# Kernel tuning notes

Hardware: AMD Instinct MI355X
Metric: run time of the kernel (lower is better)

Reference implementation:

```python
import jax, jax.numpy as jnp
import numpy as np

T = 1 << 20          # sequence length
THRESHOLD = 1e-4     # decay-reset threshold (module default)


def setup_inputs() -> dict:
    key = jax.random.key(0)
    X = jax.random.normal(key, (T,), dtype=jnp.float32)
    # stable params near module init [0.2, 0.2, 0.0, 0.0]; small w3/w4 keep the
    # quadratic recurrence bounded while exercising all terms.
    params = jnp.array([0.2, 0.2, 0.05, 0.01], dtype=jnp.float32)
    return {"X": X, "params": params}


def reference(X, params):
    dt = X.dtype
    w1 = jnp.tanh(params[0]); dtanh1 = 1.0 - w1 * w1; d2tanh1 = -2.0 * w1 * dtanh1
    w2 = jnp.tanh(params[1]); dtanh2 = 1.0 - w2 * w2; d2tanh2 = -2.0 * w2 * dtanh2
    w3, w4 = params[2], params[3]

    def step(carry, x):
        h, Jh, Hh, decay = carry  # h:(), Jh:(4,), Hh:(4,4), decay:()
        h_new = w1 * x + w2 * h + w3 * x * x + w4 * h * h
        df_dw = jnp.stack([x * dtanh1, h * dtanh2, x * x, h * h])
        df_dh = w2 + 2.0 * w4 * h
        Jh_new = df_dw + df_dh * Jh
        Hww = (jnp.zeros((4, 4), dt)
               .at[0, 0].set(x * d2tanh1)
               .at[1, 1].set(h * d2tanh2))
        g = jnp.zeros((4,), dt).at[1].set(dtanh2).at[3].set(2.0 * h)
        outer = g[:, None] * Jh[None, :]
        Hh_new = Hww + outer + outer.T + df_dh * Hh
        decay_new = decay * jnp.abs(df_dh)
        reset = decay_new < THRESHOLD
        # torch zero_() mutates storage in-place, so the appended J/H entries at a
        # reset step are also zeroed -> emit post-reset values.
        Jh_out = jnp.where(reset, jnp.zeros((4,), dt), Jh_new)
        Hh_out = jnp.where(reset, jnp.zeros((4, 4), dt), Hh_new)
        h_out = jnp.where(reset, jax.lax.stop_gradient(h_new), h_new)  # detach
        decay_out = jnp.where(reset, jnp.ones((), dt), decay_new)
        return (h_out, Jh_out, Hh_out, decay_out), (h_new, Jh_out, Hh_out)

    init = (jnp.zeros((), dt), jnp.zeros((4,), dt), jnp.zeros((4, 4), dt),
            jnp.ones((), dt))
    _, (hs, Js, Hs) = jax.lax.scan(step, init, X[:-1])
    Z = jnp.concatenate([jnp.zeros((1,), dt), hs])              # [T]
    J = jnp.concatenate([jnp.zeros((1, 4), dt), Js])            # [T, 4]
    H = jnp.concatenate([jnp.zeros((1, 4, 4), dt), Hs])         # [T, 4, 4]
    return Z, J, H
```

## Files before the change

kernel.cpp:

```cpp
#include <hip/hip_runtime.h>
#include <math.h>

#define TLEN (1 << 20)
#define SB 32
#define NSB (TLEN / SB)
#define SCB 256
#define NSCB (NSB / SCB)
#define THRESH 1e-4f
#define IDMAP 0x00FAC688u

#define WWORDS (SCB * SB + 8)
#define WPAD(i) ((i) + ((i) >> 5))
#define LDSW WPAD(WWORDS)

#pragma clang fp contract(off)


#define CHUNK55(OFS, OUTARR) {                                                 \
        const float4* xp_ = (const float4*)(X + (OFS) - 24);                   \
        float xa_[56];                                                         \
        _Pragma("unroll")                                                      \
        for (int q_ = 0; q_ < 14; ++q_) {                                      \
            float4 v_ = xp_[q_];                                               \
            xa_[4 * q_ + 0] = v_.x; xa_[4 * q_ + 1] = v_.y;                    \
            xa_[4 * q_ + 2] = v_.z; xa_[4 * q_ + 3] = v_.w;                    \
        }                                                                      \
        float h_ = 0.0f;                                                       \
        _Pragma("unroll")                                                      \
        for (int p_ = 0; p_ < 55; ++p_) {                                      \
            float x_ = xa_[p_];                                                \
            float t1_ = w1 * x_;                                               \
            float t2_ = w2 * h_;                                               \
            float s1_ = t1_ + t2_;                                             \
            float t3_ = (w3 * x_) * x_;                                        \
            float s2_ = s1_ + t3_;                                             \
            float t4_ = (w4 * h_) * h_;                                        \
            h_ = s2_ + t4_;                                                    \
            if (p_ >= 23) OUTARR[p_ - 23] = h_;                                \
        }                                                                      \
    }

__global__ void __launch_bounds__(256) k_zts(const float* __restrict__ P,
                                             const float* __restrict__ X,
                                             float* __restrict__ c,
                                             float* __restrict__ Z,
                                             unsigned int* __restrict__ L32,
                                             unsigned int* __restrict__ BT,
                                             unsigned int* __restrict__ Msk) {
#pragma clang fp contract(off)
    __shared__ float sc[4];
    __shared__ float zw[LDSW];
    __shared__ unsigned int buf[2][SCB];
    int t = threadIdx.x;
    int b = blockIdx.x;
    if (t == 0) {
        float tw1 = (float)tanh((double)P[0]);
        float tw2 = (float)tanh((double)P[1]);
        sc[0] = tw1; sc[1] = tw2; sc[2] = P[2]; sc[3] = P[3];
        if (b == 0) {
            float dt1 = 1.0f - tw1 * tw1;
            float dt2 = 1.0f - tw2 * tw2;
            c[0] = tw1; c[1] = tw2; c[2] = P[2]; c[3] = P[3];
            c[4] = dt1; c[5] = dt2;
            c[6] = (-2.0f * tw1) * dt1; c[7] = (-2.0f * tw2) * dt2;
            c[8] = 2.0f * P[3];
        }
    }
    __syncthreads();
    float w1 = sc[0], w2 = sc[1], w3 = sc[2], w4 = sc[3];
    float w42 = 2.0f * w4;
    long gi = (long)b * SCB + t;
    long o = gi * 32;
    float out[32];
    if (gi == 0) {
        float h = 0.0f;
        out[0] = 0.0f;
        for (int k = 0; k < 31; ++k) {
            float x = X[k];
            float t1 = w1 * x;
            float t2 = w2 * h;
            float s1 = t1 + t2;
            float t3 = (w3 * x) * x;
            float s2 = s1 + t3;
            float t4 = (w4 * h) * h;
            h = s2 + t4;
            out[k + 1] = h;
        }
    } else {
        CHUNK55(o, out);
    }
#pragma unroll
    for (int q = 0; q < 8; ++q)
        *(float4*)(Z + o + 4 * q) = make_float4(out[4 * q], out[4 * q + 1],
                                                out[4 * q + 2], out[4 * q + 3]);
    int rbase = t * 32 + 8;
#pragma unroll
    for (int k = 0; k < 32; ++k) zw[WPAD(rbase + k)] = out[k];
    if (t == 0 && b > 0) {
        long op = (long)b * (SCB * SB) - 32;
        float pout[32];
        CHUNK55(op, pout);
#pragma unroll
        for (int q = 0; q < 7; ++q) zw[WPAD(1 + q)] = pout[25 + q];
    }
    __syncthreads();
    unsigned int m32;
    unsigned int msk[8];
    {
        float d[8]; int last[8];
#pragma unroll
        for (int g = 0; g < 8; ++g) { d[g] = 1.0f; last[g] = -g; msk[g] = 0u; }
        if (gi == 0) {
#pragma unroll
            for (int g = 0; g < 8; ++g) last[g] = 0;
            for (int k = 0; k < 32; ++k) {
                float fa = fabsf(w2 + w42 * zw[WPAD(rbase + k)]);
#pragma unroll
                for (int g = 0; g < 8; ++g) {
                    d[g] = d[g] * fa;
                    if (d[g] < THRESH) { last[g] = k + 1; d[g] = 1.0f; msk[g] |= 1u << k; }
                }
            }
        } else {
#pragma unroll
            for (int p = 0; p < 7; ++p) {
                float fa = fabsf(w2 + w42 * zw[WPAD(rbase + p - 7)]);
#pragma unroll
                for (int g = 7 - p; g < 8; ++g) {
                    d[g] = d[g] * fa;
                    if (d[g] < THRESH) { last[g] = p - 6; d[g] = 1.0f; }
                }
            }
            for (int k = 0; k < 32; ++k) {
                float fa = fabsf(w2 + w42 * zw[WPAD(rbase + k)]);
#pragma unroll
                for (int g = 0; g < 8; ++g) {
                    d[g] = d[g] * fa;
                    if (d[g] < THRESH) { last[g] = k + 1; d[g] = 1.0f; msk[g] |= 1u << k; }
                }
            }
        }
        if (gi < NSB - 1) {
            m32 = 0;
#pragma unroll
            for (int g = 0; g < 8; ++g) {
                int delta = 32 - last[g]; if (delta > 7) delta = 7;
                m32 |= (unsigned int)delta << (3 * g);
            }
        } else {
            m32 = IDMAP;
        }
    }
    uint4* mp = (uint4*)Msk + gi * 2;
    mp[0] = make_uint4(msk[0], msk[1], msk[2], msk[3]);
    mp[1] = make_uint4(msk[4], msk[5], msk[6], msk[7]);
    buf[0][t] = m32;
    __syncthreads();
    int cur = 0;
    for (int off = 1; off < SCB; off <<= 1) {
        unsigned int hi = buf[cur][t];
        unsigned int r;
        if (t >= off) {
            unsigned int lo = buf[cur][t - off];
            r = 0;
#pragma unroll
            for (int g = 0; g < 8; ++g) {
                unsigned int lg = (lo >> (3 * g)) & 7u;
                r |= ((hi >> (3 * lg)) & 7u) << (3 * g);
            }
        } else {
            r = hi;
        }
        buf[cur ^ 1][t] = r;
        __syncthreads();
        cur ^= 1;
    }
    L32[gi] = buf[cur][t];
    if (t == SCB - 1) BT[b] = buf[cur][t];
}

__global__ void __launch_bounds__(256) k_jh7(const float* __restrict__ X,
                                             const float* __restrict__ Z,
                                             const float* __restrict__ c,
                                             const unsigned int* __restrict__ L32,
                                             const unsigned int* __restrict__ BT,
                                             const unsigned int* __restrict__ Msk,
                                             float* __restrict__ Jout,
                                             float* __restrict__ Hout) {
#pragma clang fp contract(off)
    __shared__ unsigned int sBT[NSCB];
    __shared__ unsigned int smsk[64];
    __shared__ unsigned char eL[8];
    __shared__ float zs[264];
    __shared__ float xs[264];
    __shared__ float hx[256 * 17];
    int t = threadIdx.x;
    int B = blockIdx.x;
    float w2 = c[1], dt1 = c[4], dt2 = c[5], d2t1 = c[6], d2t2 = c[7], w42 = c[8];
    long base = (long)B * 256 - 8;
    if (t < NSCB) sBT[t] = BT[t];
    if (t < 16) {
        uint4 v = ((const uint4*)Msk)[(long)B * 16 + t];
        smsk[4 * t] = v.x; smsk[4 * t + 1] = v.y;
        smsk[4 * t + 2] = v.z; smsk[4 * t + 3] = v.w;
    }
    if (t >= 128 && t < 194) {
        int s = t - 128;
        long zi = base + 4l * s;
        float4 v = make_float4(0.f, 0.f, 0.f, 0.f);
        if (zi >= 0) v = *(const float4*)(Z + zi);
        zs[4 * s] = v.x; zs[4 * s + 1] = v.y; zs[4 * s + 2] = v.z; zs[4 * s + 3] = v.w;
    } else if (t >= 194 && t < 256) {
        int s = t - 194;
        long zi = base + 4l * s;
        float4 v = make_float4(0.f, 0.f, 0.f, 0.f);
        if (zi >= 0) v = *(const float4*)(X + zi);
        xs[4 * s] = v.x; xs[4 * s + 1] = v.y; xs[4 * s + 2] = v.z; xs[4 * s + 3] = v.w;
    } else if (t >= 64 && t < 68) {
        int s = t - 64 + 62;
        long zi = base + 4l * s;
        float4 v = make_float4(0.f, 0.f, 0.f, 0.f);
        if (zi >= 0) v = *(const float4*)(X + zi);
        xs[4 * s] = v.x; xs[4 * s + 1] = v.y; xs[4 * s + 2] = v.z; xs[4 * s + 3] = v.w;
    }
    __syncthreads();
    if (t < 8) {
        int i = B * 8 + t;
        int e = 0;
        if (i > 0) {
            int bp = (i - 1) >> 8;
            unsigned int g = 0;
            for (int k = 0; k < bp; ++k) g = (sBT[k] >> (3 * g)) & 7u;
            e = (int)((L32[i - 1] >> (3 * g)) & 7u);
        }
        eL[t] = (unsigned char)e;
    }
    __syncthreads();
    long q = (long)B * 256 + t;
    int il = t >> 5;
    int j = t & 31;
    int e = (int)eL[il];
    unsigned int mask = smsk[il * 8 + e];
    unsigned int bits = mask & ((j > 0) ? ((1u << j) - 1u) : 0u);
    int a = bits ? (j + __clz(bits) - 32) : (j + e);

    float J0 = 0, J1 = 0, J2 = 0, J3 = 0;
    float H00 = 0, H01 = 0, H03 = 0, H11 = 0, H12 = 0, H13 = 0, H23 = 0, H33 = 0;
    if (a > 0) {
        long m0 = q - a + 1;
        {
            int ix = (int)(m0 - 1 - base);
            float x = xs[ix];
            float h = zs[ix];
            H00 = x * d2t1; H11 = h * d2t2;
            J0 = x * dt1; J1 = h * dt2; J2 = x * x; J3 = h * h;
        }
        for (long m = m0 + 1; m <= q; ++m) {
            int ix = (int)(m - 1 - base);
            float x = xs[ix];
            float h = zs[ix];
            float av = w2 + w42 * h;
            float g3 = 2.0f * h;
            float g1J0 = dt2 * J0, g1J1 = dt2 * J1, g1J2 = dt2 * J2, g1J3 = dt2 * J3;
            float g3J0 = g3 * J0, g3J1 = g3 * J1, g3J2 = g3 * J2, g3J3 = g3 * J3;
            float n00 = (x * d2t1) + av * H00;
            float n01 = g1J0 + av * H01;
            float n03 = g3J0 + av * H03;
            float n11 = (((h * d2t2) + g1J1) + g1J1) + av * H11;
            float n12 = g1J2 + av * H12;
            float n13 = (g1J3 + g3J1) + av * H13;
            float n23 = g3J2 + av * H23;
            float n33 = (g3J3 + g3J3) + av * H33;
            H00 = n00; H01 = n01; H03 = n03; H11 = n11;
            H12 = n12; H13 = n13; H23 = n23; H33 = n33;
            J0 = (x * dt1) + av * J0;
            J1 = (h * dt2) + av * J1;
            J2 = (x * x) + av * J2;
            J3 = (h * h) + av * J3;
        }
    }
    *((float4*)(Jout + 4 * q)) = make_float4(J0, J1, J2, J3);
    float* hr = hx + t * 17;
    hr[0]  = H00; hr[1]  = H01; hr[2]  = 0.0f; hr[3]  = H03;
    hr[4]  = H01; hr[5]  = H11; hr[6]  = H12;  hr[7]  = H13;
    hr[8]  = 0.0f; hr[9] = H12; hr[10] = 0.0f; hr[11] = H23;
    hr[12] = H03; hr[13] = H13; hr[14] = H23;  hr[15] = H33;
    __syncthreads();
    float4* Hp = (float4*)Hout + (long)B * 1024;
#pragma unroll
    for (int rr = 0; rr < 4; ++rr) {
        int f = 256 * rr + t;
        int o = f >> 2;
        int cc = (f & 3) * 4;
        const float* s = hx + o * 17 + cc;
        Hp[f] = make_float4(s[0], s[1], s[2], s[3]);
    }
}

extern "C" void kernel_launch(void* const* d_in, const int* in_sizes, int n_in,
                              void* d_out, int out_size, void* d_ws, size_t ws_size,
                              hipStream_t stream) {
    const float* X = (const float*)d_in[0];
    const float* P = (const float*)d_in[1];
    float* out = (float*)d_out;
    float* Z = out;
    float* Jout = out + (long)TLEN;
    float* Hout = out + 5l * TLEN;

    char* ws = (char*)d_ws;
    float* consts = (float*)ws;
    unsigned int* BT = (unsigned int*)(ws + 64);
    unsigned int* L32 = (unsigned int*)(ws + 1024);
    unsigned int* Msk = (unsigned int*)(ws + 1024 + (size_t)NSB * 4);

    hipLaunchKernelGGL(k_zts, dim3(NSCB), dim3(SCB), 0, stream,
                       P, X, consts, Z, L32, BT, Msk);
    hipLaunchKernelGGL(k_jh7, dim3(TLEN / 256), dim3(256), 0, stream,
                       X, Z, consts, L32, BT, Msk, Jout, Hout);
}
```

Baseline: 40.73 us.

## Split fused Z/mask/scan kernel into separate h-scan, mask-table, and block-scan kernels

The single fused kernel that computed Z with 32-element chunks, decay masks, and the block composition scan is split into three kernels. The h recurrence now runs with 8 outputs per thread after a 23-step warm-up, which gives more parallel threads but adds redundant warm-up work. The decay-mask table gets one thread per (chunk, group) and combines results with wave shuffles, and the scan becomes its own kernel. The intent is to raise parallelism and shorten per-thread serial chains, at the cost of two more launches and an extra global round trip of Z and the table.

```diff
diff --git a/kernel.cpp b/kernel.cpp
--- a/kernel.cpp
+++ b/kernel.cpp
@@ -9,74 +9,46 @@
 #define THRESH 1e-4f
 #define IDMAP 0x00FAC688u
 
-#define WWORDS (SCB * SB + 8)
-#define WPAD(i) ((i) + ((i) >> 5))
-#define LDSW WPAD(WWORDS)
-
-#pragma clang fp contract(off)
-
-
-#define CHUNK55(OFS, OUTARR) {                                                 \
-        const float4* xp_ = (const float4*)(X + (OFS) - 24);                   \
-        float xa_[56];                                                         \
-        _Pragma("unroll")                                                      \
-        for (int q_ = 0; q_ < 14; ++q_) {                                      \
-            float4 v_ = xp_[q_];                                               \
-            xa_[4 * q_ + 0] = v_.x; xa_[4 * q_ + 1] = v_.y;                    \
-            xa_[4 * q_ + 2] = v_.z; xa_[4 * q_ + 3] = v_.w;                    \
-        }                                                                      \
-        float h_ = 0.0f;                                                       \
-        _Pragma("unroll")                                                      \
-        for (int p_ = 0; p_ < 55; ++p_) {                                      \
-            float x_ = xa_[p_];                                                \
-            float t1_ = w1 * x_;                                               \
-            float t2_ = w2 * h_;                                               \
-            float s1_ = t1_ + t2_;                                             \
-            float t3_ = (w3 * x_) * x_;                                        \
-            float s2_ = s1_ + t3_;                                             \
-            float t4_ = (w4 * h_) * h_;                                        \
-            h_ = s2_ + t4_;                                                    \
-            if (p_ >= 23) OUTARR[p_ - 23] = h_;                                \
-        }                                                                      \
-    }
-
-__global__ void __launch_bounds__(256) k_zts(const float* __restrict__ P,
-                                             const float* __restrict__ X,
-                                             float* __restrict__ c,
-                                             float* __restrict__ Z,
-                                             unsigned int* __restrict__ L32,
-                                             unsigned int* __restrict__ BT,
-                                             unsigned int* __restrict__ Msk) {
+#pragma clang fp contract(off)
+
+
+__global__ void __launch_bounds__(256) k_hscan(const float* __restrict__ P,
+                                               const float* __restrict__ X,
+                                               float* __restrict__ c,
+                                               float* __restrict__ Z) {
 #pragma clang fp contract(off)
     __shared__ float sc[4];
-    __shared__ float zw[LDSW];
-    __shared__ unsigned int buf[2][SCB];
-    int t = threadIdx.x;
-    int b = blockIdx.x;
-    if (t == 0) {
-        float tw1 = (float)tanh((double)P[0]);
-        float tw2 = (float)tanh((double)P[1]);
-        sc[0] = tw1; sc[1] = tw2; sc[2] = P[2]; sc[3] = P[3];
-        if (b == 0) {
-            float dt1 = 1.0f - tw1 * tw1;
-            float dt2 = 1.0f - tw2 * tw2;
-            c[0] = tw1; c[1] = tw2; c[2] = P[2]; c[3] = P[3];
+    if (threadIdx.x == 0) {
+        float w1 = (float)tanh((double)P[0]);
+        float w2 = (float)tanh((double)P[1]);
+        sc[0] = w1; sc[1] = w2; sc[2] = P[2]; sc[3] = P[3];
+        if (blockIdx.x == 0) {
+            float dt1 = 1.0f - w1 * w1;
+            float dt2 = 1.0f - w2 * w2;
+            c[0] = w1; c[1] = w2; c[2] = P[2]; c[3] = P[3];
             c[4] = dt1; c[5] = dt2;
-            c[6] = (-2.0f * tw1) * dt1; c[7] = (-2.0f * tw2) * dt2;
+            c[6] = (-2.0f * w1) * dt1; c[7] = (-2.0f * w2) * dt2;
             c[8] = 2.0f * P[3];
         }
     }
     __syncthreads();
     float w1 = sc[0], w2 = sc[1], w3 = sc[2], w4 = sc[3];
-    float w42 = 2.0f * w4;
-    long gi = (long)b * SCB + t;
-    long o = gi * 32;
-    float out[32];
-    if (gi == 0) {
+    long j = blockIdx.x * (long)blockDim.x + threadIdx.x;
+    long o = j * 8;
+    if (j >= 3) {
+        const float4* xp = (const float4*)(X + o - 24);
+        float xa[32];
+#pragma unroll
+        for (int q = 0; q < 8; ++q) {
+            float4 v = xp[q];
+            xa[4 * q + 0] = v.x; xa[4 * q + 1] = v.y;
+            xa[4 * q + 2] = v.z; xa[4 * q + 3] = v.w;
+        }
         float h = 0.0f;
-        out[0] = 0.0f;
-        for (int k = 0; k < 31; ++k) {
-            float x = X[k];
+        float out[8];
+#pragma unroll
+        for (int p = 0; p < 31; ++p) {
+            float x = xa[p];
             float t1 = w1 * x;
             float t2 = w2 * h;
             float s1 = t1 + t2;
@@ -84,77 +56,71 @@
             float s2 = s1 + t3;
             float t4 = (w4 * h) * h;
             h = s2 + t4;
-            out[k + 1] = h;
-        }
+            if (p >= 23) out[p - 23] = h;
+        }
+        *(float4*)(Z + o) = make_float4(out[0], out[1], out[2], out[3]);
+        *(float4*)(Z + o + 4) = make_float4(out[4], out[5], out[6], out[7]);
     } else {
-        CHUNK55(o, out);
-    }
-#pragma unroll
-    for (int q = 0; q < 8; ++q)
-        *(float4*)(Z + o + 4 * q) = make_float4(out[4 * q], out[4 * q + 1],
-                                                out[4 * q + 2], out[4 * q + 3]);
-    int rbase = t * 32 + 8;
-#pragma unroll
-    for (int k = 0; k < 32; ++k) zw[WPAD(rbase + k)] = out[k];
-    if (t == 0 && b > 0) {
-        long op = (long)b * (SCB * SB) - 32;
-        float pout[32];
-        CHUNK55(op, pout);
-#pragma unroll
-        for (int q = 0; q < 7; ++q) zw[WPAD(1 + q)] = pout[25 + q];
-    }
-    __syncthreads();
-    unsigned int m32;
-    unsigned int msk[8];
-    {
-        float d[8]; int last[8];
-#pragma unroll
-        for (int g = 0; g < 8; ++g) { d[g] = 1.0f; last[g] = -g; msk[g] = 0u; }
-        if (gi == 0) {
-#pragma unroll
-            for (int g = 0; g < 8; ++g) last[g] = 0;
-            for (int k = 0; k < 32; ++k) {
-                float fa = fabsf(w2 + w42 * zw[WPAD(rbase + k)]);
-#pragma unroll
-                for (int g = 0; g < 8; ++g) {
-                    d[g] = d[g] * fa;
-                    if (d[g] < THRESH) { last[g] = k + 1; d[g] = 1.0f; msk[g] |= 1u << k; }
-                }
-            }
-        } else {
-#pragma unroll
-            for (int p = 0; p < 7; ++p) {
-                float fa = fabsf(w2 + w42 * zw[WPAD(rbase + p - 7)]);
-#pragma unroll
-                for (int g = 7 - p; g < 8; ++g) {
-                    d[g] = d[g] * fa;
-                    if (d[g] < THRESH) { last[g] = p - 6; d[g] = 1.0f; }
-                }
-            }
-            for (int k = 0; k < 32; ++k) {
-                float fa = fabsf(w2 + w42 * zw[WPAD(rbase + k)]);
-#pragma unroll
-                for (int g = 0; g < 8; ++g) {
-                    d[g] = d[g] * fa;
-                    if (d[g] < THRESH) { last[g] = k + 1; d[g] = 1.0f; msk[g] |= 1u << k; }
-                }
-            }
-        }
-        if (gi < NSB - 1) {
-            m32 = 0;
-#pragma unroll
-            for (int g = 0; g < 8; ++g) {
-                int delta = 32 - last[g]; if (delta > 7) delta = 7;
-                m32 |= (unsigned int)delta << (3 * g);
-            }
-        } else {
-            m32 = IDMAP;
-        }
-    }
-    uint4* mp = (uint4*)Msk + gi * 2;
-    mp[0] = make_uint4(msk[0], msk[1], msk[2], msk[3]);
-    mp[1] = make_uint4(msk[4], msk[5], msk[6], msk[7]);
-    buf[0][t] = m32;
+        long b = o - 24; if (b < 0) b = 0;
+        long tend = o + 7;
+        float h = 0.0f;
+        if (o == 0) Z[0] = 0.0f;
+        for (long t = b; t < tend; ++t) {
+            float x = X[t];
+            float t1 = w1 * x;
+            float t2 = w2 * h;
+            float s1 = t1 + t2;
+            float t3 = (w3 * x) * x;
+            float s2 = s1 + t3;
+            float t4 = (w4 * h) * h;
+            h = s2 + t4;
+            if (t + 1 >= o) Z[t + 1] = h;
+        }
+    }
+}
+
+__global__ void __launch_bounds__(256) k_tabm(const float* __restrict__ c,
+                                              const float* __restrict__ Z,
+                                              unsigned int* __restrict__ tab32,
+                                              unsigned int* __restrict__ Msk) {
+#pragma clang fp contract(off)
+    long tid = blockIdx.x * (long)blockDim.x + threadIdx.x;
+    if (tid >= (long)NSB * 8) return;
+    int i = (int)(tid >> 3);
+    int g = (int)(tid & 7);
+    float w2 = c[1], w42 = c[8];
+    long ci = (long)i * SB;
+    long start = ci - g; if (start < 0) start = 0;
+    long end = ci + SB;
+    float d = 1.0f;
+    long last = start;
+    unsigned int msk = 0u;
+    for (long m = start + 1; m <= end; ++m) {
+        float a = w2 + w42 * Z[m - 1];
+        d = d * fabsf(a);
+        if (d < THRESH) {
+            last = m; d = 1.0f;
+            if (m > ci) msk |= 1u << (int)(m - ci - 1);
+        }
+    }
+    Msk[(long)i * 8 + g] = msk;
+    if (i < NSB - 1) {
+        long delta = end - last; if (delta > 7) delta = 7;
+        unsigned int v = (unsigned int)delta << (3 * g);
+        v |= __shfl_xor(v, 1);
+        v |= __shfl_xor(v, 2);
+        v |= __shfl_xor(v, 4);
+        if (g == 0) tab32[i] = v;
+    }
+}
+
+__global__ void __launch_bounds__(256) k_scanA(const unsigned int* __restrict__ tab32,
+                                               unsigned int* __restrict__ L32,
+                                               unsigned int* __restrict__ BT) {
+    __shared__ unsigned int buf[2][SCB];
+    int t = threadIdx.x;
+    long gi = (long)blockIdx.x * SCB + t;
+    buf[0][t] = (gi < NSB - 1) ? tab32[gi] : IDMAP;
     __syncthreads();
     int cur = 0;
     for (int off = 1; off < SCB; off <<= 1) {
@@ -176,7 +142,7 @@
         cur ^= 1;
     }
     L32[gi] = buf[cur][t];
-    if (t == SCB - 1) BT[b] = buf[cur][t];
+    if (t == SCB - 1) BT[blockIdx.x] = buf[cur][t];
 }
 
 __global__ void __launch_bounds__(256) k_jh7(const float* __restrict__ X,
@@ -310,11 +276,16 @@
     char* ws = (char*)d_ws;
     float* consts = (float*)ws;
     unsigned int* BT = (unsigned int*)(ws + 64);
-    unsigned int* L32 = (unsigned int*)(ws + 1024);
-    unsigned int* Msk = (unsigned int*)(ws + 1024 + (size_t)NSB * 4);
-
-    hipLaunchKernelGGL(k_zts, dim3(NSCB), dim3(SCB), 0, stream,
-                       P, X, consts, Z, L32, BT, Msk);
+    unsigned int* tab32 = (unsigned int*)(ws + 1024);
+    unsigned int* L32 = (unsigned int*)(ws + 1024 + (size_t)NSB * 4);
+    unsigned int* Msk = (unsigned int*)(ws + 1024 + 2 * (size_t)NSB * 4);
+
+    hipLaunchKernelGGL(k_hscan, dim3(TLEN / 8 / 256), dim3(256), 0, stream,
+                       P, X, consts, Z);
+    hipLaunchKernelGGL(k_tabm, dim3(NSB * 8 / 256), dim3(256), 0, stream,
+                       consts, Z, tab32, Msk);
+    hipLaunchKernelGGL(k_scanA, dim3(NSCB), dim3(SCB), 0, stream,
+                       tab32, L32, BT);
     hipLaunchKernelGGL(k_jh7, dim3(TLEN / 256), dim3(256), 0, stream,
                        X, Z, consts, L32, BT, Msk, Jout, Hout);
 }
```

After: 40.23 us, median of 2. Within noise of the previous version (-1.2%).
